# Performance work log

Hardware: AMD Instinct MI355X
Metric: run time of the kernel (lower is better)

## Reference

```python
import jax, jax.numpy as jnp
import numpy as np

VEC_DIM = 3          # Cl(3,0): 3 positive-signature basis vectors
BASIS_DIM = 1 << VEC_DIM  # 8 basis blades
BATCH, IN_F, OUT_F = 512, 512, 512


def cayley_table(n: int = VEC_DIM) -> np.ndarray:
    """Geometric-product tensor G[i, j, k] for Cl(n,0) with blades as bitmasks.
    e_a * e_b = sign(a,b) * e_{a XOR b}; Euclidean metric so e_i^2 = +1.
    Only 2^(2n) of the 2^(3n) entries are nonzero (highly sparse)."""
    dim = 1 << n
    G = np.zeros((dim, dim, dim), dtype=np.float32)
    for a in range(dim):
        for b in range(dim):
            # sign from counting transpositions to bring blade product to canonical order
            swaps, t = 0, a >> 1
            while t:
                swaps += bin(t & b).count("1")
                t >>= 1
            G[a, b, a ^ b] = -1.0 if (swaps & 1) else 1.0
    return G


def setup_inputs() -> dict:
    key = jax.random.key(0)
    kx, kw, kb = jax.random.split(key, 3)
    x = jax.random.normal(kx, (BATCH, IN_F, BASIS_DIM), dtype=jnp.float32)
    W = jax.random.normal(kw, (IN_F, OUT_F, BASIS_DIM), dtype=jnp.float32)
    b = jax.random.normal(kb, (OUT_F, BASIS_DIM), dtype=jnp.float32)
    G = jnp.asarray(cayley_table())  # exact Cl(3,0) geometric-product tensor
    return {"x": x, "W": W, "b": b, "G": G}


def reference(x, W, b, G):
    # out[b,o,k] = sum_{i,j,p} G[i,j,k] * x[b,p,i] * W[p,o,j]  (+ bias)
    out = jnp.einsum("ijk,bpi,poj->bok", G, x, W)
    return out + b
```

## Files before the change

### kernel.cpp

```cpp
#include <hip/hip_runtime.h>
#include <hip/hip_bf16.h>
#include <stdint.h>

typedef __attribute__((ext_vector_type(8))) short short8;
typedef __attribute__((ext_vector_type(4))) float floatx4;

__device__ __forceinline__ unsigned short bfu(float a) {
    return __builtin_bit_cast(unsigned short, __float2bfloat16(a));
}
__device__ __forceinline__ uint32_t pkbf(float a, float b) {
    return (uint32_t)bfu(a) | ((uint32_t)bfu(b) << 16);
}


__global__ __launch_bounds__(256) void pack_x(
    const float* __restrict__ x, unsigned short* __restrict__ Abuf)
{
    __shared__ unsigned short TX[4][1024];
    const int b = blockIdx.x;
    const int t = threadIdx.x;
    const float4* src = (const float4*)(x + ((size_t)b * 512 + 2 * t) * 8);
    float4 f[4] = {src[0], src[1], src[2], src[3]};
    #pragma unroll
    for (int pp = 0; pp < 2; ++pp) {
        const float a0 = f[2*pp].x, a1 = f[2*pp].y, a2 = f[2*pp].z, a3 = f[2*pp].w;
        const float a4 = f[2*pp+1].x, a5 = f[2*pp+1].y, a6 = f[2*pp+1].z, a7 = f[2*pp+1].w;
        const int c = 4 * t + 2 * pp;
        TX[0][c] = bfu(a0 + a4); TX[0][c+1] = bfu(a1 - a5);
        TX[1][c] = bfu(a3 + a7); TX[1][c+1] = bfu(a6 - a2);
        TX[2][c] = bfu(a1 + a5); TX[2][c+1] = bfu(a0 - a4);
        TX[3][c] = bfu(a6 + a2); TX[3][c+1] = bfu(a7 - a3);
    }
    __syncthreads();
    const int tr = t >> 6, off = (t & 63) * 16;
    uint4* dst = (uint4*)(Abuf + (size_t)(2*b + (tr >> 1)) * 2048 + (tr & 1) * 1024 + off);
    const uint4* s4 = (const uint4*)&TX[tr][off];
    dst[0] = s4[0]; dst[1] = s4[1];
}

__global__ __launch_bounds__(256) void pack_w(
    const float* __restrict__ W, unsigned short* __restrict__ BT)
{
    const int wb = blockIdx.x;
    const int pbase = (wb & 7) * 64;
    const int o0 = (wb >> 3) * 16;
    const int t = threadIdx.x;
    const int pc = t & 15;
    const int o = o0 + (t >> 4);
    float R[4][2][2], I[4][2][2];
    #pragma unroll
    for (int u = 0; u < 4; ++u) {
        const float4* src = (const float4*)(W + ((size_t)(pbase + pc * 4 + u) * 512 + o) * 8);
        float4 lo = src[0], hi = src[1];
        R[u][0][0] = lo.x + hi.x;  I[u][0][0] = lo.w + hi.w;
        R[u][0][1] = lo.y - hi.y;  I[u][0][1] = hi.z - lo.z;
        R[u][1][0] = lo.y + hi.y;  I[u][1][0] = hi.z + lo.z;
        R[u][1][1] = lo.x - hi.x;  I[u][1][1] = hi.w - lo.w;
    }
    const int kbase = 2 * pbase + pc * 8;
    #pragma unroll
    for (int part = 0; part < 2; ++part)
        #pragma unroll
        for (int pN = 0; pN < 2; ++pN)
            #pragma unroll
            for (int c = 0; c < 2; ++c) {
                uint4 v; uint32_t* vv = (uint32_t*)&v;
                #pragma unroll
                for (int u = 0; u < 4; ++u) {
                    const float v0 = (part == 0) ? (pN ? I[u][0][c] : R[u][0][c])
                                                 : (pN ? R[u][0][c] : -I[u][0][c]);
                    const float v1 = (part == 0) ? (pN ? I[u][1][c] : R[u][1][c])
                                                 : (pN ? R[u][1][c] : -I[u][1][c]);
                    vv[u] = pkbf(v0, v1);
                }
                const int n = 4 * o + 2 * pN + c;
                *(uint4*)&BT[(size_t)n * 2048 + part * 1024 + kbase] = v;
            }
}

#define GLL(src, dstoff) \
    __builtin_amdgcn_global_load_lds((const __attribute__((address_space(1))) uint32_t*)(src), \
        (__attribute__((address_space(3))) uint32_t*)(smem + (dstoff)), 16, 0, 0)

__global__ __launch_bounds__(512, 2) void iso_gemm(
    const unsigned short* __restrict__ AB,
    const unsigned short* __restrict__ BB,
    const float* __restrict__ bias,
    float*       __restrict__ out)
{
    __shared__ __align__(16) unsigned char smem[98304];
    const int t = threadIdx.x, lane = t & 63, wave = t >> 6;
    const int wn = wave & 1;
    const int g  = wave >> 1;
    const int l15 = lane & 15, q = lane >> 4;

    const int lin = blockIdx.y * 16 + blockIdx.x;
    const int xcd = lin & 7, sx = lin >> 3;
    const int tn = (xcd & 3) * 4 + (sx & 3);
    const int tm = (xcd >> 2) * 8 + (sx >> 2);
    const int m0 = tm * 64, v0 = tn * 128;

    const unsigned short* a_srcs[2]; int a_dst[2];
    #pragma unroll
    for (int i = 0; i < 2; ++i) {
        const int sl = (wave * 2 + i) * 64 + lane;
        const int row = sl >> 4, slot = sl & 15, chunk = slot ^ (row & 7);
        a_srcs[i] = AB + (size_t)(m0 + row) * 2048 + chunk * 8;
        a_dst[i] = (wave * 2 + i) * 1024;
    }
    const unsigned short* b_srcs[4]; int b_dst[4];
    #pragma unroll
    for (int i = 0; i < 4; ++i) {
        const int sl = (wave * 4 + i) * 64 + lane;
        const int row = sl >> 4, slot = sl & 15, chunk = slot ^ (row & 7);
        b_srcs[i] = BB + (size_t)(v0 + row) * 2048 + chunk * 8;
        b_dst[i] = 16384 + (wave * 4 + i) * 1024;
    }

    const int chunk = g * 4 + q;
    const int slot = chunk ^ (l15 & 7);
    const int a_off = l15 * 256 + slot * 16;
    const int b_off = 16384 + (wn * 64 + l15) * 256 + slot * 16;

    floatx4 acc[4][4] = {};

    #pragma unroll
    for (int i = 0; i < 2; ++i) GLL(a_srcs[i], a_dst[i]);
    #pragma unroll
    for (int i = 0; i < 4; ++i) GLL(b_srcs[i], b_dst[i]);

    for (int kt = 0; kt < 16; ++kt) {
        __syncthreads();
        const int cur = (kt & 1) * 49152;
        if (kt + 1 < 16) {
            const int nxt = ((kt + 1) & 1) * 49152;
            const int poff = (kt + 1) * 128;
            #pragma unroll
            for (int i = 0; i < 2; ++i) GLL(a_srcs[i] + poff, nxt + a_dst[i]);
            #pragma unroll
            for (int i = 0; i < 4; ++i) GLL(b_srcs[i] + poff, nxt + b_dst[i]);
        }
        short8 af[4], bf[4];
        #pragma unroll
        for (int fm = 0; fm < 4; ++fm)
            af[fm] = *(const short8*)&smem[cur + a_off + fm * 4096];
        #pragma unroll
        for (int fn = 0; fn < 4; ++fn)
            bf[fn] = *(const short8*)&smem[cur + b_off + fn * 4096];
        #pragma unroll
        for (int fm = 0; fm < 4; ++fm)
            #pragma unroll
            for (int fn = 0; fn < 4; ++fn)
                acc[fm][fn] = __builtin_amdgcn_mfma_f32_16x16x32_bf16(
                    af[fm], bf[fn], acc[fm][fn], 0, 0, 0);
    }

    __syncthreads();
    float* red = (float*)smem;
    if (g >= 2) {
        float* r = red + (wn * 2 + (g - 2)) * 4096;
        #pragma unroll
        for (int f = 0; f < 16; ++f)
            *(floatx4*)&r[f * 256 + lane * 4] = acc[f >> 2][f & 3];
    }
    __syncthreads();
    if (g < 2) {
        const float* r = red + (wn * 2 + g) * 4096;
        #pragma unroll
        for (int f = 0; f < 16; ++f)
            acc[f >> 2][f & 3] += *(const floatx4*)&r[f * 256 + lane * 4];
    }
    __syncthreads();
    if (g == 1) {
        float* r = red + wn * 4096;
        #pragma unroll
        for (int f = 0; f < 16; ++f)
            *(floatx4*)&r[f * 256 + lane * 4] = acc[f >> 2][f & 3];
    }
    __syncthreads();
    float* Cf = (float*)(smem + 32768);
    if (g == 0) {
        const float* r = red + wn * 4096;
        #pragma unroll
        for (int f = 0; f < 16; ++f)
            acc[f >> 2][f & 3] += *(const floatx4*)&r[f * 256 + lane * 4];
        #pragma unroll
        for (int fm = 0; fm < 4; ++fm)
            #pragma unroll
            for (int fn = 0; fn < 4; ++fn)
                #pragma unroll
                for (int rr = 0; rr < 4; ++rr) {
                    const int row = fm * 16 + q * 4 + rr;
                    const int col = wn * 64 + fn * 16 + l15;
                    Cf[row * 130 + col] = acc[fm][fn][rr];
                }
    }
    __syncthreads();
    const int b0 = m0 >> 1, o0 = v0 >> 2;
    #pragma unroll
    for (int rnd = 0; rnd < 2; ++rnd) {
        const int pi = rnd * 512 + t;
        const int o_l = pi & 31, b_l = pi >> 5;
        const float* r0 = &Cf[(2 * b_l) * 130 + 4 * o_l];
        const float* r1 = r0 + 130;
        const float Cr00 = r0[0], Cr01 = r0[1], Ci00 = r0[2], Ci01 = r0[3];
        const float Cr10 = r1[0], Cr11 = r1[1], Ci10 = r1[2], Ci11 = r1[3];
        const float a0 = 0.5f * (Cr00 + Cr11), a7 = 0.5f * (Ci00 + Ci11);
        const float a4 = 0.5f * (Cr00 - Cr11), a3 = 0.5f * (Ci00 - Ci11);
        const float a1 = 0.5f * (Cr01 + Cr10), a6 = 0.5f * (Ci01 + Ci10);
        const float a2 = 0.5f * (Ci10 - Ci01), a5 = 0.5f * (Cr10 - Cr01);
        const int o = o0 + o_l, b = b0 + b_l;
        const float* bp = bias + o * 8;
        float4 lo = {a0 + bp[0], a1 + bp[1], a2 + bp[2], a3 + bp[3]};
        float4 hi = {a4 + bp[4], a5 + bp[5], a6 + bp[6], a7 + bp[7]};
        float* op = out + ((size_t)b * 512 + o) * 8;
        *(float4*)op = lo;
        *(float4*)(op + 4) = hi;
    }
}

__device__ __align__(16) const uint32_t SGN[4][4] = {
    {0x00000000u, 0x80000000u, 0x80000000u, 0x80008000u},
    {0x80000000u, 0x00000000u, 0x00000000u, 0x00008000u},
    {0x80000000u, 0x80008000u, 0x00000000u, 0x80000000u},
    {0x00000000u, 0x00008000u, 0x80000000u, 0x00000000u},
};
__device__ __forceinline__ uint32_t swap16(uint32_t a) { return (a >> 16) | (a << 16); }
__device__ __forceinline__ uint4 xperm2(uint4 v, int kp) {
    const bool s1 = (kp & 1) != 0;
    uint32_t x1 = s1 ? v.y : v.x, y1 = s1 ? v.x : v.y, z1 = s1 ? v.w : v.z, w1 = s1 ? v.z : v.w;
    const bool s2 = (kp & 2) != 0;
    uint4 r; r.x = s2 ? z1 : x1; r.y = s2 ? w1 : y1; r.z = s2 ? x1 : z1; r.w = s2 ? y1 : w1;
    return r;
}
__global__ __launch_bounds__(512) void gp_linear_legacy(
    const float* __restrict__ xg_raw, const float* __restrict__ wg,
    const float* __restrict__ bias, float* __restrict__ out)
{
    __shared__ __align__(16) unsigned short As[128 * 64];
    __shared__ __align__(16) unsigned short Bs[8 * 64 * 8];
    const int t = threadIdx.x, lane = t & 63, wave = t >> 6;
    const int m0 = blockIdx.y * 128, n0 = blockIdx.x * 64;
    const int ap = t & 7, akp = (t >> 3) & 3, ab = t >> 5, ak0 = akp * 2;
    const uint4 mask = *(const uint4*)SGN[akp];
    const int wm = wave & 3, wnn = wave >> 2, l15 = lane & 15, q = lane >> 4;
    floatx4 acc[2][2] = {};
    const float4* xg = (const float4*)xg_raw;
    const int bg0 = m0 >> 3;
    float4 ax0, ax1, bw0, bw1;
    {
        const size_t aidx = ((size_t)(bg0 + ab) * 512 + ap) * 2;
        ax0 = xg[aidx]; ax1 = xg[aidx + 1];
        const float* gsrc = wg + (((size_t)wave * 512 + n0) << 3) + (lane << 3);
        bw0 = *(const float4*)gsrc; bw1 = *(const float4*)(gsrc + 4);
    }
    for (int kt = 0; kt < 64; ++kt) {
        __syncthreads();
        {
            uint4 v;
            v.x = pkbf(ax0.x, ax0.y); v.y = pkbf(ax0.z, ax0.w);
            v.z = pkbf(ax1.x, ax1.y); v.w = pkbf(ax1.z, ax1.w);
            uint4 pk = xperm2(v, akp), r0, p1, r1;
            r0.x = pk.x ^ mask.x; r0.y = pk.y ^ mask.y; r0.z = pk.z ^ mask.z; r0.w = pk.w ^ mask.w;
            p1.x = swap16(pk.x); p1.y = swap16(pk.y); p1.z = swap16(pk.z); p1.w = swap16(pk.w);
            r1.x = p1.x ^ mask.x; r1.y = p1.y ^ mask.y; r1.z = p1.z ^ mask.z; r1.w = p1.w ^ mask.w;
            const int row0 = ab * 8 + ak0;
            *(uint4*)&As[row0 * 64 + ((ap ^ ak0) << 3)] = r0;
            *(uint4*)&As[(row0 + 1) * 64 + ((ap ^ (ak0 + 1)) << 3)] = r1;
        }
        {
            uint4 b0;
            b0.x = pkbf(bw0.x, bw0.y); b0.y = pkbf(bw0.z, bw0.w);
            b0.z = pkbf(bw1.x, bw1.y); b0.w = pkbf(bw1.z, bw1.w);
            *(uint4*)&Bs[t << 3] = b0;
        }
        __syncthreads();
        if (kt + 1 < 64) {
            const int p0n = (kt + 1) * 8;
            const size_t aidx = ((size_t)(bg0 + ab) * 512 + p0n + ap) * 2;
            ax0 = xg[aidx]; ax1 = xg[aidx + 1];
            const float* gsrc = wg + (((size_t)(p0n + wave) * 512 + n0) << 3) + (lane << 3);
            bw0 = *(const float4*)gsrc; bw1 = *(const float4*)(gsrc + 4);
        }
        #pragma unroll
        for (int ks = 0; ks < 2; ++ks) {
            const int cb = ks * 4 + q;
            short8 a[2], bfr[2];
            #pragma unroll
            for (int fm = 0; fm < 2; ++fm) {
                const int row = wm * 32 + fm * 16 + l15;
                a[fm] = *(const short8*)&As[row * 64 + ((cb ^ (l15 & 7)) << 3)];
            }
            #pragma unroll
            for (int fn = 0; fn < 2; ++fn) {
                const int nl = wnn * 32 + fn * 16 + l15;
                bfr[fn] = *(const short8*)&Bs[((cb * 64) + nl) << 3];
            }
            #pragma unroll
            for (int fm = 0; fm < 2; ++fm)
                #pragma unroll
                for (int fn = 0; fn < 2; ++fn)
                    acc[fm][fn] = __builtin_amdgcn_mfma_f32_16x16x32_bf16(a[fm], bfr[fn], acc[fm][fn], 0, 0, 0);
        }
    }
    #pragma unroll
    for (int fm = 0; fm < 2; ++fm)
        #pragma unroll
        for (int fn = 0; fn < 2; ++fn) {
            const int n = n0 + wnn * 32 + fn * 16 + l15;
            #pragma unroll
            for (int r = 0; r < 4; ++r) {
                const int m = m0 + wm * 32 + fm * 16 + q * 4 + r;
                const int bi = m >> 3, k = m & 7;
                out[(size_t)bi * 4096 + n * 8 + k] = acc[fm][fn][r] + bias[n * 8 + k];
            }
        }
}

extern "C" void kernel_launch(void* const* d_in, const int* in_sizes, int n_in,
                              void* d_out, int out_size, void* d_ws, size_t ws_size,
                              hipStream_t stream) {
    const float* x  = (const float*)d_in[0];
    const float* W  = (const float*)d_in[1];
    const float* bb = (const float*)d_in[2];
    float* out = (float*)d_out;

    const size_t abytes = (size_t)1024 * 2048 * sizeof(unsigned short);
    const size_t bbytes = (size_t)2048 * 2048 * sizeof(unsigned short);
    if (ws_size >= abytes + bbytes) {
        unsigned short* Abuf = (unsigned short*)d_ws;
        unsigned short* Bbuf = (unsigned short*)((char*)d_ws + abytes);
        pack_x<<<512, 256, 0, stream>>>(x, Abuf);
        pack_w<<<256, 256, 0, stream>>>(W, Bbuf);
        iso_gemm<<<dim3(16, 16), 512, 0, stream>>>(Abuf, Bbuf, bb, out);
    } else {
        gp_linear_legacy<<<dim3(8, 32), dim3(512), 0, stream>>>(x, W, bb, out);
    }
}
```

Baseline: 94.05 us.

## Merge pack kernels and load GEMM operands directly into registers

Fuses pack_x and pack_w into one pack_all launch, which removes one kernel launch and lets the two packing jobs overlap. The W-pack thread mapping is swapped so adjacent threads read adjacent outputs. The GEMM no longer stages tiles through LDS with async global-to-LDS loads. Each wave now loads its bf16 fragments straight from global memory into double-buffered registers, and the split-K reduction is simplified to one LDS round. This drops the LDS staging and per-tile barriers, but the global loads become strided per lane, and the launch-bounds occupancy hint is relaxed.

```diff
diff --git a/kernel.cpp b/kernel.cpp
--- a/kernel.cpp
+++ b/kernel.cpp
@@ -13,76 +13,70 @@
 }
 
 
-__global__ __launch_bounds__(256) void pack_x(
-    const float* __restrict__ x, unsigned short* __restrict__ Abuf)
+__global__ __launch_bounds__(256) void pack_all(
+    const float* __restrict__ x, const float* __restrict__ W,
+    unsigned short* __restrict__ Abuf, unsigned short* __restrict__ BT)
 {
-    __shared__ unsigned short TX[4][1024];
-    const int b = blockIdx.x;
     const int t = threadIdx.x;
-    const float4* src = (const float4*)(x + ((size_t)b * 512 + 2 * t) * 8);
-    float4 f[4] = {src[0], src[1], src[2], src[3]};
-    #pragma unroll
-    for (int pp = 0; pp < 2; ++pp) {
-        const float a0 = f[2*pp].x, a1 = f[2*pp].y, a2 = f[2*pp].z, a3 = f[2*pp].w;
-        const float a4 = f[2*pp+1].x, a5 = f[2*pp+1].y, a6 = f[2*pp+1].z, a7 = f[2*pp+1].w;
-        const int c = 4 * t + 2 * pp;
-        TX[0][c] = bfu(a0 + a4); TX[0][c+1] = bfu(a1 - a5);
-        TX[1][c] = bfu(a3 + a7); TX[1][c+1] = bfu(a6 - a2);
-        TX[2][c] = bfu(a1 + a5); TX[2][c+1] = bfu(a0 - a4);
-        TX[3][c] = bfu(a6 + a2); TX[3][c+1] = bfu(a7 - a3);
-    }
-    __syncthreads();
-    const int tr = t >> 6, off = (t & 63) * 16;
-    uint4* dst = (uint4*)(Abuf + (size_t)(2*b + (tr >> 1)) * 2048 + (tr & 1) * 1024 + off);
-    const uint4* s4 = (const uint4*)&TX[tr][off];
-    dst[0] = s4[0]; dst[1] = s4[1];
-}
-
-__global__ __launch_bounds__(256) void pack_w(
-    const float* __restrict__ W, unsigned short* __restrict__ BT)
-{
-    const int wb = blockIdx.x;
-    const int pbase = (wb & 7) * 64;
-    const int o0 = (wb >> 3) * 16;
-    const int t = threadIdx.x;
-    const int pc = t & 15;
-    const int o = o0 + (t >> 4);
-    float R[4][2][2], I[4][2][2];
-    #pragma unroll
-    for (int u = 0; u < 4; ++u) {
-        const float4* src = (const float4*)(W + ((size_t)(pbase + pc * 4 + u) * 512 + o) * 8);
-        float4 lo = src[0], hi = src[1];
-        R[u][0][0] = lo.x + hi.x;  I[u][0][0] = lo.w + hi.w;
-        R[u][0][1] = lo.y - hi.y;  I[u][0][1] = hi.z - lo.z;
-        R[u][1][0] = lo.y + hi.y;  I[u][1][0] = hi.z + lo.z;
-        R[u][1][1] = lo.x - hi.x;  I[u][1][1] = hi.w - lo.w;
-    }
-    const int kbase = 2 * pbase + pc * 8;
-    #pragma unroll
-    for (int part = 0; part < 2; ++part)
-        #pragma unroll
-        for (int pN = 0; pN < 2; ++pN)
-            #pragma unroll
-            for (int c = 0; c < 2; ++c) {
-                uint4 v; uint32_t* vv = (uint32_t*)&v;
+    if (blockIdx.x < 512) {
+        __shared__ unsigned short TX[4][1024];
+        const int b = blockIdx.x;
+        const float4* src = (const float4*)(x + ((size_t)b * 512 + 2 * t) * 8);
+        float4 f[4] = {src[0], src[1], src[2], src[3]};
+        #pragma unroll
+        for (int pp = 0; pp < 2; ++pp) {
+            const float a0 = f[2*pp].x, a1 = f[2*pp].y, a2 = f[2*pp].z, a3 = f[2*pp].w;
+            const float a4 = f[2*pp+1].x, a5 = f[2*pp+1].y, a6 = f[2*pp+1].z, a7 = f[2*pp+1].w;
+            const int c = 4 * t + 2 * pp;
+            TX[0][c] = bfu(a0 + a4); TX[0][c+1] = bfu(a1 - a5);
+            TX[1][c] = bfu(a3 + a7); TX[1][c+1] = bfu(a6 - a2);
+            TX[2][c] = bfu(a1 + a5); TX[2][c+1] = bfu(a0 - a4);
+            TX[3][c] = bfu(a6 + a2); TX[3][c+1] = bfu(a7 - a3);
+        }
+        __syncthreads();
+        const int tr = t >> 6, off = (t & 63) * 16;
+        uint4* dst = (uint4*)(Abuf + (size_t)(2*b + (tr >> 1)) * 2048 + (tr & 1) * 1024 + off);
+        const uint4* s4 = (const uint4*)&TX[tr][off];
+        dst[0] = s4[0]; dst[1] = s4[1];
+    } else {
+        const int wb = blockIdx.x - 512;
+        const int pbase = (wb & 7) * 64;
+        const int o0 = (wb >> 3) * 16;
+        const int o = o0 + (t & 15);
+        const int pc = t >> 4;
+        float R[4][2][2], I[4][2][2];
+        #pragma unroll
+        for (int u = 0; u < 4; ++u) {
+            const float4* src = (const float4*)(W + ((size_t)(pbase + pc * 4 + u) * 512 + o) * 8);
+            float4 lo = src[0], hi = src[1];
+            R[u][0][0] = lo.x + hi.x;  I[u][0][0] = lo.w + hi.w;
+            R[u][0][1] = lo.y - hi.y;  I[u][0][1] = hi.z - lo.z;
+            R[u][1][0] = lo.y + hi.y;  I[u][1][0] = hi.z + lo.z;
+            R[u][1][1] = lo.x - hi.x;  I[u][1][1] = hi.w - lo.w;
+        }
+        const int kbase = 2 * pbase + pc * 8;
+        #pragma unroll
+        for (int part = 0; part < 2; ++part)
+            #pragma unroll
+            for (int pN = 0; pN < 2; ++pN)
                 #pragma unroll
-                for (int u = 0; u < 4; ++u) {
-                    const float v0 = (part == 0) ? (pN ? I[u][0][c] : R[u][0][c])
-                                                 : (pN ? R[u][0][c] : -I[u][0][c]);
-                    const float v1 = (part == 0) ? (pN ? I[u][1][c] : R[u][1][c])
-                                                 : (pN ? R[u][1][c] : -I[u][1][c]);
-                    vv[u] = pkbf(v0, v1);
+                for (int c = 0; c < 2; ++c) {
+                    uint4 v; uint32_t* vv = (uint32_t*)&v;
+                    #pragma unroll
+                    for (int u = 0; u < 4; ++u) {
+                        const float v0 = (part == 0) ? (pN ? I[u][0][c] : R[u][0][c])
+                                                     : (pN ? R[u][0][c] : -I[u][0][c]);
+                        const float v1 = (part == 0) ? (pN ? I[u][1][c] : R[u][1][c])
+                                                     : (pN ? R[u][1][c] : -I[u][1][c]);
+                        vv[u] = pkbf(v0, v1);
+                    }
+                    const int n = 4 * o + 2 * pN + c;
+                    *(uint4*)&BT[(size_t)n * 2048 + part * 1024 + kbase] = v;
                 }
-                const int n = 4 * o + 2 * pN + c;
-                *(uint4*)&BT[(size_t)n * 2048 + part * 1024 + kbase] = v;
-            }
-}
-
-#define GLL(src, dstoff) \
-    __builtin_amdgcn_global_load_lds((const __attribute__((address_space(1))) uint32_t*)(src), \
-        (__attribute__((address_space(3))) uint32_t*)(smem + (dstoff)), 16, 0, 0)
-
-__global__ __launch_bounds__(512, 2) void iso_gemm(
+    }
+}
+
+__global__ __launch_bounds__(512) void iso_gemm2(
     const unsigned short* __restrict__ AB,
     const unsigned short* __restrict__ BB,
     const float* __restrict__ bias,
@@ -100,90 +94,62 @@
     const int tm = (xcd >> 2) * 8 + (sx >> 2);
     const int m0 = tm * 64, v0 = tn * 128;
 
-    const unsigned short* a_srcs[2]; int a_dst[2];
+    const unsigned short* arow[4];
+    const unsigned short* brow[4];
     #pragma unroll
-    for (int i = 0; i < 2; ++i) {
-        const int sl = (wave * 2 + i) * 64 + lane;
-        const int row = sl >> 4, slot = sl & 15, chunk = slot ^ (row & 7);
-        a_srcs[i] = AB + (size_t)(m0 + row) * 2048 + chunk * 8;
-        a_dst[i] = (wave * 2 + i) * 1024;
-    }
-    const unsigned short* b_srcs[4]; int b_dst[4];
+    for (int f = 0; f < 4; ++f) {
+        arow[f] = AB + (size_t)(m0 + f * 16 + l15) * 2048;
+        brow[f] = BB + (size_t)(v0 + wn * 64 + f * 16 + l15) * 2048;
+    }
+    const int kbase = g * 512 + q * 8;
+
+    floatx4 acc[4][4] = {};
+    short8 abuf[2][4], bbuf[2][4];
+
     #pragma unroll
-    for (int i = 0; i < 4; ++i) {
-        const int sl = (wave * 4 + i) * 64 + lane;
-        const int row = sl >> 4, slot = sl & 15, chunk = slot ^ (row & 7);
-        b_srcs[i] = BB + (size_t)(v0 + row) * 2048 + chunk * 8;
-        b_dst[i] = 16384 + (wave * 4 + i) * 1024;
-    }
-
-    const int chunk = g * 4 + q;
-    const int slot = chunk ^ (l15 & 7);
-    const int a_off = l15 * 256 + slot * 16;
-    const int b_off = 16384 + (wn * 64 + l15) * 256 + slot * 16;
-
-    floatx4 acc[4][4] = {};
-
-    #pragma unroll
-    for (int i = 0; i < 2; ++i) GLL(a_srcs[i], a_dst[i]);
-    #pragma unroll
-    for (int i = 0; i < 4; ++i) GLL(b_srcs[i], b_dst[i]);
-
-    for (int kt = 0; kt < 16; ++kt) {
-        __syncthreads();
-        const int cur = (kt & 1) * 49152;
-        if (kt + 1 < 16) {
-            const int nxt = ((kt + 1) & 1) * 49152;
-            const int poff = (kt + 1) * 128;
-            #pragma unroll
-            for (int i = 0; i < 2; ++i) GLL(a_srcs[i] + poff, nxt + a_dst[i]);
-            #pragma unroll
-            for (int i = 0; i < 4; ++i) GLL(b_srcs[i] + poff, nxt + b_dst[i]);
-        }
-        short8 af[4], bf[4];
-        #pragma unroll
-        for (int fm = 0; fm < 4; ++fm)
-            af[fm] = *(const short8*)&smem[cur + a_off + fm * 4096];
-        #pragma unroll
-        for (int fn = 0; fn < 4; ++fn)
-            bf[fn] = *(const short8*)&smem[cur + b_off + fn * 4096];
+    for (int f = 0; f < 4; ++f) {
+        abuf[0][f] = *(const short8*)(arow[f] + kbase);
+        bbuf[0][f] = *(const short8*)(brow[f] + kbase);
+    }
+    #pragma unroll 2
+    for (int it = 0; it < 16; ++it) {
+        const int cb = it & 1, nb = cb ^ 1;
+        if (it < 15) {
+            const int kk = kbase + (it + 1) * 32;
+            #pragma unroll
+            for (int f = 0; f < 4; ++f) {
+                abuf[nb][f] = *(const short8*)(arow[f] + kk);
+                bbuf[nb][f] = *(const short8*)(brow[f] + kk);
+            }
+        }
         #pragma unroll
         for (int fm = 0; fm < 4; ++fm)
             #pragma unroll
             for (int fn = 0; fn < 4; ++fn)
                 acc[fm][fn] = __builtin_amdgcn_mfma_f32_16x16x32_bf16(
-                    af[fm], bf[fn], acc[fm][fn], 0, 0, 0);
+                    abuf[cb][fm], bbuf[cb][fn], acc[fm][fn], 0, 0, 0);
     }
 
     __syncthreads();
-    float* red = (float*)smem;
-    if (g >= 2) {
-        float* r = red + (wn * 2 + (g - 2)) * 4096;
+    if (g > 0) {
+        float* r = (float*)(smem + ((g - 1) * 2 + wn) * 16384);
         #pragma unroll
         for (int f = 0; f < 16; ++f)
             *(floatx4*)&r[f * 256 + lane * 4] = acc[f >> 2][f & 3];
     }
     __syncthreads();
-    if (g < 2) {
-        const float* r = red + (wn * 2 + g) * 4096;
-        #pragma unroll
-        for (int f = 0; f < 16; ++f)
-            acc[f >> 2][f & 3] += *(const floatx4*)&r[f * 256 + lane * 4];
+    if (g == 0) {
+        #pragma unroll
+        for (int gg = 1; gg < 4; ++gg) {
+            const float* r = (const float*)(smem + ((gg - 1) * 2 + wn) * 16384);
+            #pragma unroll
+            for (int f = 0; f < 16; ++f)
+                acc[f >> 2][f & 3] += *(const floatx4*)&r[f * 256 + lane * 4];
+        }
     }
     __syncthreads();
-    if (g == 1) {
-        float* r = red + wn * 4096;
-        #pragma unroll
-        for (int f = 0; f < 16; ++f)
-            *(floatx4*)&r[f * 256 + lane * 4] = acc[f >> 2][f & 3];
-    }
-    __syncthreads();
-    float* Cf = (float*)(smem + 32768);
+    float* Cf = (float*)smem;
     if (g == 0) {
-        const float* r = red + wn * 4096;
-        #pragma unroll
-        for (int f = 0; f < 16; ++f)
-            acc[f >> 2][f & 3] += *(const floatx4*)&r[f * 256 + lane * 4];
         #pragma unroll
         for (int fm = 0; fm < 4; ++fm)
             #pragma unroll
@@ -330,9 +296,8 @@
     if (ws_size >= abytes + bbytes) {
         unsigned short* Abuf = (unsigned short*)d_ws;
         unsigned short* Bbuf = (unsigned short*)((char*)d_ws + abytes);
-        pack_x<<<512, 256, 0, stream>>>(x, Abuf);
-        pack_w<<<256, 256, 0, stream>>>(W, Bbuf);
-        iso_gemm<<<dim3(16, 16), 512, 0, stream>>>(Abuf, Bbuf, bb, out);
+        pack_all<<<768, 256, 0, stream>>>(x, W, Abuf, Bbuf);
+        iso_gemm2<<<dim3(16, 16), 512, 0, stream>>>(Abuf, Bbuf, bb, out);
     } else {
         gp_linear_legacy<<<dim3(8, 32), dim3(512), 0, stream>>>(x, W, bb, out);
     }
```

After: 107.5 us. 1.14x slower.
